# Kernel optimization log

Hardware: AMD Instinct MI355X
Metric: run time of the kernel (lower is better)

## Reference

```python
import jax, jax.numpy as jnp
import numpy as np

B, S, D = 2, 2048, 2048
H, KV, HD = 16, 8, 128
N_REP = H // KV


def _rotate_half(x):
    x1, x2 = x[..., : x.shape[-1] // 2], x[..., x.shape[-1] // 2 :]
    return jnp.concatenate((-x2, x1), axis=-1)


def setup_inputs() -> dict:
    key = jax.random.key(0)
    ks = jax.random.split(key, 5)
    x = jax.random.normal(ks[0], (B, S, D), dtype=jnp.float32)
    # rotary tables (llama-style): inv_freq over half dims, duplicated
    inv_freq = 1.0 / (10000.0 ** (jnp.arange(0, HD, 2, dtype=jnp.float32) / HD))
    t = jnp.arange(S, dtype=jnp.float32)
    freqs = jnp.outer(t, inv_freq)                      # [S, HD/2]
    emb = jnp.concatenate((freqs, freqs), axis=-1)      # [S, HD]
    cos, sin = jnp.cos(emb), jnp.sin(emb)
    sc = 0.02
    Wq = jax.random.normal(ks[1], (D, H * HD), dtype=jnp.float32) * sc
    Wk = jax.random.normal(ks[2], (D, KV * HD), dtype=jnp.float32) * sc
    Wv = jax.random.normal(ks[3], (D, KV * HD), dtype=jnp.float32) * sc
    Wo = jax.random.normal(ks[4], (H * HD, D), dtype=jnp.float32) * sc
    return {"x": x, "cos": cos, "sin": sin, "Wq": Wq, "Wk": Wk, "Wv": Wv, "Wo": Wo}


def reference(x, cos, sin, Wq, Wk, Wv, Wo):
    b, s, _ = x.shape
    q = (x @ Wq).reshape(b, s, H, HD)
    k = (x @ Wk).reshape(b, s, KV, HD)
    v = (x @ Wv).reshape(b, s, KV, HD)
    # RoPE (broadcast over batch and heads; unsqueeze_dim=2 layout [b,s,h,d])
    c = cos[None, :, None, :]
    sn = sin[None, :, None, :]
    q = q * c + _rotate_half(q) * sn
    k = k * c + _rotate_half(k) * sn
    # GQA expansion (repeat_kv == interleaved repeat along head dim)
    k = jnp.repeat(k, N_REP, axis=2)
    v = jnp.repeat(v, N_REP, axis=2)
    scale = HD ** -0.5
    # causal attention (single-rank ring attention == one causal flash block)
    scores = jnp.einsum("bqhd,bkhd->bhqk", q, k) * scale
    mask = jnp.tril(jnp.ones((s, s), dtype=bool))
    scores = jnp.where(mask[None, None], scores, -jnp.inf)
    probs = jax.nn.softmax(scores, axis=-1)
    attn = jnp.einsum("bhqk,bkhd->bqhd", probs, v).reshape(b, s, H * HD)
    return attn @ Wo
```

## Files before the change

kernel.cpp:

```cpp
#include <hip/hip_runtime.h>


typedef __bf16 bf16;
typedef __bf16 bf16x4 __attribute__((ext_vector_type(4)));
typedef __bf16 bf16x8 __attribute__((ext_vector_type(8)));
typedef float floatx4 __attribute__((ext_vector_type(4)));

#define AS1(p) ((const __attribute__((address_space(1))) void*)(p))
#define AS3(p) ((__attribute__((address_space(3))) void*)(p))

__device__ __forceinline__ void load16(const void* g, void* l) {
  __builtin_amdgcn_global_load_lds(AS1(g), AS3(l), 16, 0, 0);
}

__device__ __forceinline__ void phase_barrier() {
  asm volatile("" ::: "memory");
  __builtin_amdgcn_sched_barrier(0);
  __builtin_amdgcn_s_barrier();
  __builtin_amdgcn_sched_barrier(0);
  asm volatile("" ::: "memory");
}

__global__ __launch_bounds__(256) void cvt_kernel(const float* __restrict__ in,
                                                  bf16* __restrict__ out, int n4) {
  int i = blockIdx.x * blockDim.x + threadIdx.x;
  if (i >= n4) return;
  float4 v = ((const float4*)in)[i];
  bf16x4 o = {(bf16)v.x, (bf16)v.y, (bf16)v.z, (bf16)v.w};
  ((bf16x4*)out)[i] = o;
}

__global__ __launch_bounds__(256) void wtrans_kernel(
    const float* __restrict__ Wq, const float* __restrict__ Wk,
    const float* __restrict__ Wv, const float* __restrict__ Wo,
    bf16* __restrict__ WqkvT, bf16* __restrict__ WoT) {
  __shared__ float tile[32][33];
  const int wid = blockIdx.z;
  const float* src = wid == 0 ? Wq : wid == 1 ? Wk : wid == 2 ? Wv : Wo;
  bf16* dst = wid == 0 ? WqkvT
            : wid == 1 ? WqkvT + 2048ull * 2048
            : wid == 2 ? WqkvT + 3072ull * 2048
                       : WoT;
  const int ncols = (wid == 1 || wid == 2) ? 1024 : 2048;
  const int c0 = blockIdx.x * 32, r0 = blockIdx.y * 32;
  if (c0 >= ncols) return;
  const int tx = threadIdx.x & 31, ty = threadIdx.x >> 5;
#pragma unroll
  for (int i = 0; i < 4; i++) {
    int ri = ty + i * 8;
    tile[ri][tx] = src[(long)(r0 + ri) * ncols + c0 + tx];
  }
  __syncthreads();
#pragma unroll
  for (int i = 0; i < 4; i++) {
    int ci = ty + i * 8;
    dst[(long)(c0 + ci) * 2048 + r0 + tx] = (bf16)tile[tx][ci];
  }
}

__global__ __launch_bounds__(256) void transpose_bf16(
    const bf16* __restrict__ in, bf16* __restrict__ out,
    int ldi, int ldo, long ibs, long obs) {
  __shared__ bf16 tile[32][33];
  const long ib = ibs * blockIdx.z, ob = obs * blockIdx.z;
  const int c0 = blockIdx.x * 32, r0 = blockIdx.y * 32;
  const int tx = threadIdx.x & 31, ty = threadIdx.x >> 5;
#pragma unroll
  for (int i = 0; i < 4; i++) {
    int ri = ty + i * 8;
    tile[ri][tx] = in[ib + (long)(r0 + ri) * ldi + c0 + tx];
  }
  __syncthreads();
#pragma unroll
  for (int i = 0; i < 4; i++) {
    int ci = ty + i * 8;
    out[ob + (long)(c0 + ci) * ldo + r0 + tx] = tile[tx][ci];
  }
}

template <typename CT>
__global__ __launch_bounds__(512, 2) void gemm256(
    const bf16* __restrict__ A, const bf16* __restrict__ Bt, CT* __restrict__ C,
    int M, int N, int K) {
  __shared__ __align__(1024) char smem[131072];
  const int tid = threadIdx.x;
  const int wave = tid >> 6, lane = tid & 63;
  const int quad = lane >> 4, l16 = lane & 15;
  const int wm = wave >> 2, wn = wave & 3;
  const int m0 = blockIdx.y * 256, n0 = blockIdx.x * 256;

  const int srow = (wave >> 1) * 16 + (lane >> 2);
  const int skcol = (wave & 1) * 32 + (((lane & 3) * 8) ^ ((lane & 32) ? 16 : 0));
  const int sblk = wave * 1024;

  const int qoff = (quad * 16) ^ ((l16 & 8) << 2);
  const int aoff = wm * 16384 + l16 * 64 + qoff;
  const int boff = 32768 + (wn >> 1) * 16384 + (wn & 1) * 8192 + l16 * 64 + qoff;

  auto stageA = [&](int kt, int h, int buf) {
    const bf16* g = A + (size_t)(m0 + h * 128 + srow) * K + kt * 64 + skcol;
    char* d = smem + buf * 65536 + h * 16384 + sblk;
    load16(g, d);
    load16(g + (size_t)64 * K, d + 8192);
  };
  auto stageB = [&](int kt, int h, int buf) {
    const bf16* g = Bt + (size_t)(n0 + h * 128 + srow) * K + kt * 64 + skcol;
    char* d = smem + buf * 65536 + 32768 + h * 16384 + sblk;
    load16(g, d);
    load16(g + (size_t)64 * K, d + 8192);
  };
  auto rdA = [&](int buf, int fr, int ks) {
    return *(const bf16x8*)(smem + buf * 65536 + aoff + (fr * 2 + ks) * 1024);
  };
  auto rdB = [&](int buf, int fc, int ks) {
    return *(const bf16x8*)(smem + buf * 65536 + boff + (fc * 2 + ks) * 1024);
  };

  floatx4 acc[8][4] = {};

  const int nkt = K >> 6;
  const int niter = nkt >> 1;

  stageB(0, 0, 0); stageB(0, 1, 0);
  stageA(0, 0, 0); stageA(0, 1, 0);
  stageB(1, 0, 1); stageB(1, 1, 1);
  asm volatile("s_waitcnt vmcnt(4)" ::: "memory");
  phase_barrier();

  for (int it = 0; it < niter; ++it) {
    const int T = 2 * it;
    const bool morek = (it < niter - 1);
#pragma unroll
    for (int c = 0; c < 2; ++c) {
      const int buf = c;
      const int tA = T + 1 + c;
      const int tB = T + 2 + c;
      const bool stA = (c == 0) || morek;

      bf16x8 a[4][2], b01[2][2], b23[2][2];

#pragma unroll
      for (int fr = 0; fr < 4; ++fr)
#pragma unroll
        for (int ks = 0; ks < 2; ++ks) a[fr][ks] = rdA(buf, fr, ks);
#pragma unroll
      for (int fc = 0; fc < 2; ++fc)
#pragma unroll
        for (int ks = 0; ks < 2; ++ks) b01[fc][ks] = rdB(buf, fc, ks);
      if (stA) stageA(tA, 0, buf ^ 1);
      phase_barrier();
      __builtin_amdgcn_s_setprio(1);
#pragma unroll
      for (int ks = 0; ks < 2; ++ks)
#pragma unroll
        for (int fr = 0; fr < 4; ++fr)
#pragma unroll
          for (int fc = 0; fc < 2; ++fc)
            acc[fr][fc] = __builtin_amdgcn_mfma_f32_16x16x32_bf16(
                a[fr][ks], b01[fc][ks], acc[fr][fc], 0, 0, 0);
      __builtin_amdgcn_s_setprio(0);
      phase_barrier();

#pragma unroll
      for (int fc = 0; fc < 2; ++fc)
#pragma unroll
        for (int ks = 0; ks < 2; ++ks) b23[fc][ks] = rdB(buf, 2 + fc, ks);
      if (stA) stageA(tA, 1, buf ^ 1);
      phase_barrier();
      __builtin_amdgcn_s_setprio(1);
#pragma unroll
      for (int ks = 0; ks < 2; ++ks)
#pragma unroll
        for (int fr = 0; fr < 4; ++fr)
#pragma unroll
          for (int fc = 0; fc < 2; ++fc)
            acc[fr][2 + fc] = __builtin_amdgcn_mfma_f32_16x16x32_bf16(
                a[fr][ks], b23[fc][ks], acc[fr][2 + fc], 0, 0, 0);
      __builtin_amdgcn_s_setprio(0);
      phase_barrier();

#pragma unroll
      for (int fr = 0; fr < 4; ++fr)
#pragma unroll
        for (int ks = 0; ks < 2; ++ks) a[fr][ks] = rdA(buf, 4 + fr, ks);
      if (morek) stageB(tB, 0, buf);
      phase_barrier();
      __builtin_amdgcn_s_setprio(1);
#pragma unroll
      for (int ks = 0; ks < 2; ++ks)
#pragma unroll
        for (int fr = 0; fr < 4; ++fr)
#pragma unroll
          for (int fc = 0; fc < 2; ++fc)
            acc[4 + fr][2 + fc] = __builtin_amdgcn_mfma_f32_16x16x32_bf16(
                a[fr][ks], b23[fc][ks], acc[4 + fr][2 + fc], 0, 0, 0);
      __builtin_amdgcn_s_setprio(0);
      phase_barrier();

      if (morek) stageB(tB, 1, buf);
      if (morek)
        asm volatile("s_waitcnt vmcnt(4)" ::: "memory");
      else
        asm volatile("s_waitcnt vmcnt(0)" ::: "memory");
      phase_barrier();
      __builtin_amdgcn_s_setprio(1);
#pragma unroll
      for (int ks = 0; ks < 2; ++ks)
#pragma unroll
        for (int fr = 0; fr < 4; ++fr)
#pragma unroll
          for (int fc = 0; fc < 2; ++fc)
            acc[4 + fr][fc] = __builtin_amdgcn_mfma_f32_16x16x32_bf16(
                a[fr][ks], b01[fc][ks], acc[4 + fr][fc], 0, 0, 0);
      __builtin_amdgcn_s_setprio(0);
      phase_barrier();
    }
  }

#pragma unroll
  for (int fr = 0; fr < 8; ++fr)
#pragma unroll
    for (int fc = 0; fc < 4; ++fc)
#pragma unroll
      for (int r = 0; r < 4; ++r) {
        int row = m0 + wm * 128 + fr * 16 + quad * 4 + r;
        int col = n0 + wn * 64 + fc * 16 + l16;
        C[(size_t)row * N + col] = (CT)acc[fr][fc][r];
      }
}

__global__ void rope_kernel(bf16* __restrict__ QKV, const float* __restrict__ cosb,
                            const float* __restrict__ sinb) {
  int idx = blockIdx.x * blockDim.x + threadIdx.x;
  if (idx >= 6291456) return;
  int nh, nhs, offc;
  if (idx < 4194304) { nh = 16; nhs = 4; offc = 0; }
  else { idx -= 4194304; nh = 8; nhs = 3; offc = 2048; }
  int d = idx & 63;
  int rest = idx >> 6;
  int hh = rest & (nh - 1);
  int bs = rest >> nhs;
  int s = bs & 2047;
  size_t base = (size_t)bs * 4096 + offc + hh * 128;
  float c0 = cosb[s * 128 + d];
  float c1 = cosb[s * 128 + d + 64];
  float s0 = sinb[s * 128 + d];
  float s1 = sinb[s * 128 + d + 64];
  float x0 = (float)QKV[base + d];
  float x1 = (float)QKV[base + d + 64];
  QKV[base + d] = (bf16)(x0 * c0 - x1 * s0);
  QKV[base + d + 64] = (bf16)(x1 * c1 + x0 * s1);
}


template <bool MASK>
__device__ __forceinline__ void attn_step32(
    const bf16* Kc, const bf16* Vc, bf16* Pw, const bf16x8 (&aq)[4],
    const bf16x8& ones, floatx4 (&oacc)[8], floatx4& lacc,
    int k0, int q0w, int l16, int quad) {
  floatx4 sacc[4] = {};
  __builtin_amdgcn_s_setprio(1);
#pragma unroll
  for (int ks = 0; ks < 4; ks++)
#pragma unroll
    for (int j = 0; j < 4; j++) {
      int row = j * 16 + l16;
      bf16x8 bk = *(const bf16x8*)(Kc + row * 128 + (((ks * 4 + quad) ^ (row & 15)) * 8));
      sacc[j] = __builtin_amdgcn_mfma_f32_16x16x32_bf16(aq[ks], bk, sacc[j], 0, 0, 0);
    }
  __builtin_amdgcn_s_setprio(0);
  const float C = 0.12752188659023044f;
#pragma unroll
  for (int r = 0; r < 4; r++) {
    int row = quad * 4 + r;
#pragma unroll
    for (int j = 0; j < 4; j++) {
      float p = exp2f(sacc[j][r] * C);
      if (MASK) {
        int key = k0 + j * 16 + l16;
        if (key > q0w + row) p = 0.f;
      }
      int col = j * 16 + l16;
      Pw[row * 64 + (((col >> 3) ^ (row & 7)) * 8) + (col & 7)] = (bf16)p;
    }
  }
  __builtin_amdgcn_s_setprio(1);
#pragma unroll
  for (int ks = 0; ks < 2; ks++) {
    bf16x8 ap = *(const bf16x8*)(Pw + l16 * 64 + (((ks * 4 + quad) ^ (l16 & 7)) * 8));
    lacc = __builtin_amdgcn_mfma_f32_16x16x32_bf16(ap, ones, lacc, 0, 0, 0);
#pragma unroll
    for (int j = 0; j < 8; j++) {
      int vr = j * 16 + l16;
      bf16x8 bv = *(const bf16x8*)(Vc + vr * 64 + (((ks * 4 + quad) ^ (vr & 7)) * 8));
      oacc[j] = __builtin_amdgcn_mfma_f32_16x16x32_bf16(ap, bv, oacc[j], 0, 0, 0);
    }
  }
  __builtin_amdgcn_s_setprio(0);
}

__global__ __launch_bounds__(512, 4) void flash_kernel(
    const bf16* __restrict__ QKV, const bf16* __restrict__ Vt, bf16* __restrict__ O) {
  __shared__ __align__(1024) char smem[81920];
  const int tid = threadIdx.x;
  const int wave = tid >> 6, lane = tid & 63, quad = lane >> 4, l16 = lane & 15;
  const int wbase = tid & ~63;
  const int hloc = wave & 1, rgroup = wave >> 1;
  bf16* Pw = (bf16*)(smem + 65536) + wave * 1024;
  bf16x8 ones;
#pragma unroll
  for (int e = 0; e < 8; e++) ones[e] = (bf16)1.0f;

  const int w = blockIdx.x;
  const int side = w & 1, kvh = (w >> 1) & 7, b = (w >> 4) & 1, g = w >> 5;
  const int qt = side ? 31 - g : g;
  const int h = kvh * 2 + hloc;
  const int q0 = qt * 64;
  const int nkt = qt + 1;

#pragma unroll
  for (int u = 0; u < 4; u++) {
    int gg = u * 512 + tid;
    int row = gg >> 4, cc = gg & 15;
    const bf16* gp = QKV + (size_t)(b * 2048 + q0 + (row & 63)) * 4096 +
                     (kvh * 2 + (row >> 6)) * 128 + ((cc ^ (row & 15)) * 8);
    load16(gp, smem + (u * 512 + wbase) * 16);
  }
  asm volatile("s_waitcnt vmcnt(0)" ::: "memory");
  phase_barrier();
  bf16x8 aq[4];
  {
    int qr = hloc * 64 + rgroup * 16 + l16;
#pragma unroll
    for (int ks = 0; ks < 4; ks++)
      aq[ks] = *(const bf16x8*)((const bf16*)smem + qr * 128 +
                                (((ks * 4 + quad) ^ (qr & 15)) * 8));
  }
  __syncthreads();

  auto stageKV = [&](int kt, int nb) {
    char* kd = smem + nb * 16384;
    char* vd = smem + 32768 + nb * 16384;
#pragma unroll
    for (int u = 0; u < 2; u++) {
      int gg = u * 512 + tid;
      int krow = gg >> 4, kcc = gg & 15;
      const bf16* kp = QKV + (size_t)(b * 2048 + kt * 64 + krow) * 4096 + 2048 +
                       kvh * 128 + ((kcc ^ (krow & 15)) * 8);
      load16(kp, kd + (u * 512 + wbase) * 16);
      int vrow = gg >> 3, vcc = gg & 7;
      const bf16* vp = Vt + (size_t)(b * 1024 + kvh * 128 + vrow) * 2048 + kt * 64 +
                       ((vcc ^ (vrow & 7)) * 8);
      load16(vp, vd + (u * 512 + wbase) * 16);
    }
  };

  stageKV(0, 0);

  floatx4 oacc[8] = {};
  floatx4 lacc = {};
  const int q0w = q0 + rgroup * 16;

  for (int kt = 0; kt < nkt; kt++) {
    const int cur = kt & 1;
    if (kt + 1 < nkt) {
      stageKV(kt + 1, cur ^ 1);
      asm volatile("s_waitcnt vmcnt(4)" ::: "memory");
    } else {
      asm volatile("s_waitcnt vmcnt(0)" ::: "memory");
    }
    phase_barrier();
    const bf16* Kc = (const bf16*)(smem + cur * 16384);
    const bf16* Vc = (const bf16*)(smem + 32768 + cur * 16384);
    if (kt == nkt - 1)
      attn_step32<true>(Kc, Vc, Pw, aq, ones, oacc, lacc, kt * 64, q0w, l16, quad);
    else
      attn_step32<false>(Kc, Vc, Pw, aq, ones, oacc, lacc, kt * 64, q0w, l16, quad);
    phase_barrier();
  }

  float rl[4];
#pragma unroll
  for (int r = 0; r < 4; r++) rl[r] = 1.0f / lacc[r];
#pragma unroll
  for (int j = 0; j < 8; j++)
#pragma unroll
    for (int r = 0; r < 4; r++) {
      int s = q0w + quad * 4 + r;
      O[(size_t)(b * 2048 + s) * 2048 + h * 128 + j * 16 + l16] =
          (bf16)(oacc[j][r] * rl[r]);
    }
}

extern "C" void kernel_launch(void* const* d_in, const int* in_sizes, int n_in,
                              void* d_out, int out_size, void* d_ws, size_t ws_size,
                              hipStream_t stream) {
  (void)in_sizes; (void)n_in; (void)out_size; (void)ws_size;
  const float* x    = (const float*)d_in[0];
  const float* cosb = (const float*)d_in[1];
  const float* sinb = (const float*)d_in[2];
  const float* Wq   = (const float*)d_in[3];
  const float* Wk   = (const float*)d_in[4];
  const float* Wv   = (const float*)d_in[5];
  const float* Wo   = (const float*)d_in[6];
  float* out = (float*)d_out;

  char* ws = (char*)d_ws;
  size_t off = 0;
  auto alloc = [&](size_t bytes) { void* p = ws + off; off += bytes; return p; };
  bf16* xb    = (bf16*)alloc(4096ull * 2048 * 2);
  bf16* WqkvT = (bf16*)alloc(4096ull * 2048 * 2);
  bf16* WoT   = (bf16*)alloc(2048ull * 2048 * 2);
  bf16* QKV   = (bf16*)alloc(4096ull * 4096 * 2);
  bf16* Vtb   = (bf16*)alloc(2048ull * 2048 * 2);
  bf16* Ab    = (bf16*)alloc(4096ull * 2048 * 2);

  cvt_kernel<<<8192, 256, 0, stream>>>(x, xb, 2097152);

  wtrans_kernel<<<dim3(64, 64, 4), 256, 0, stream>>>(Wq, Wk, Wv, Wo, WqkvT, WoT);

  gemm256<bf16><<<dim3(16, 16), 512, 0, stream>>>(xb, WqkvT, QKV, 4096, 4096, 2048);

  rope_kernel<<<24576, 256, 0, stream>>>(QKV, cosb, sinb);

  transpose_bf16<<<dim3(32, 64, 2), 256, 0, stream>>>(
      QKV + 3072, Vtb, 4096, 2048, 2048ll * 4096, 1024ll * 2048);

  flash_kernel<<<dim3(512, 1, 1), 512, 0, stream>>>(QKV, Vtb, Ab);

  gemm256<float><<<dim3(8, 16), 512, 0, stream>>>(Ab, WoT, out, 4096, 2048, 2048);
}
```

Before: 342.1 us.

## Merge prep and mid kernels, use 256x128 tiles for output projection

Combines the x conversion and weight transpose into one launch, and RoPE plus the V transpose into another, which removes two kernel launches and their gaps. It also adds a 256x128-tile GEMM for the output projection, giving 256 blocks instead of 128 so more CUs are busy on the 4096x2048 output. The smaller tile lowers per-block data reuse and uses launch bounds of one block per CU.

```diff
diff --git a/kernel.cpp b/kernel.cpp
--- a/kernel.cpp
+++ b/kernel.cpp
@@ -21,28 +21,30 @@
   asm volatile("" ::: "memory");
 }
 
-__global__ __launch_bounds__(256) void cvt_kernel(const float* __restrict__ in,
-                                                  bf16* __restrict__ out, int n4) {
-  int i = blockIdx.x * blockDim.x + threadIdx.x;
-  if (i >= n4) return;
-  float4 v = ((const float4*)in)[i];
-  bf16x4 o = {(bf16)v.x, (bf16)v.y, (bf16)v.z, (bf16)v.w};
-  ((bf16x4*)out)[i] = o;
-}
-
-__global__ __launch_bounds__(256) void wtrans_kernel(
-    const float* __restrict__ Wq, const float* __restrict__ Wk,
-    const float* __restrict__ Wv, const float* __restrict__ Wo,
+__global__ __launch_bounds__(256) void prep_kernel(
+    const float* __restrict__ x, const float* __restrict__ Wq,
+    const float* __restrict__ Wk, const float* __restrict__ Wv,
+    const float* __restrict__ Wo, bf16* __restrict__ xb,
     bf16* __restrict__ WqkvT, bf16* __restrict__ WoT) {
   __shared__ float tile[32][33];
-  const int wid = blockIdx.z;
+  const int bi = blockIdx.x;
+  if (bi < 8192) {
+    int i = bi * 256 + threadIdx.x;
+    float4 v = ((const float4*)x)[i];
+    bf16x4 o = {(bf16)v.x, (bf16)v.y, (bf16)v.z, (bf16)v.w};
+    ((bf16x4*)xb)[i] = o;
+    return;
+  }
+  const int i2 = bi - 8192;
+  const int wid = i2 >> 12;
+  const int r0 = ((i2 >> 6) & 63) * 32;
+  const int c0 = (i2 & 63) * 32;
   const float* src = wid == 0 ? Wq : wid == 1 ? Wk : wid == 2 ? Wv : Wo;
   bf16* dst = wid == 0 ? WqkvT
             : wid == 1 ? WqkvT + 2048ull * 2048
             : wid == 2 ? WqkvT + 3072ull * 2048
                        : WoT;
   const int ncols = (wid == 1 || wid == 2) ? 1024 : 2048;
-  const int c0 = blockIdx.x * 32, r0 = blockIdx.y * 32;
   if (c0 >= ncols) return;
   const int tx = threadIdx.x & 31, ty = threadIdx.x >> 5;
 #pragma unroll
@@ -58,23 +60,49 @@
   }
 }
 
-__global__ __launch_bounds__(256) void transpose_bf16(
-    const bf16* __restrict__ in, bf16* __restrict__ out,
-    int ldi, int ldo, long ibs, long obs) {
+__global__ __launch_bounds__(256) void mid_kernel(
+    bf16* __restrict__ QKV, const float* __restrict__ cosb,
+    const float* __restrict__ sinb, bf16* __restrict__ Vtb) {
   __shared__ bf16 tile[32][33];
-  const long ib = ibs * blockIdx.z, ob = obs * blockIdx.z;
-  const int c0 = blockIdx.x * 32, r0 = blockIdx.y * 32;
+  const int bi = blockIdx.x;
+  if (bi < 24576) {
+    int idx = bi * 256 + threadIdx.x;
+    int nh, nhs, offc;
+    if (idx < 4194304) { nh = 16; nhs = 4; offc = 0; }
+    else { idx -= 4194304; nh = 8; nhs = 3; offc = 2048; }
+    int d = idx & 63;
+    int rest = idx >> 6;
+    int hh = rest & (nh - 1);
+    int bs = rest >> nhs;
+    int s = bs & 2047;
+    size_t base = (size_t)bs * 4096 + offc + hh * 128;
+    float c0 = cosb[s * 128 + d];
+    float c1 = cosb[s * 128 + d + 64];
+    float s0 = sinb[s * 128 + d];
+    float s1 = sinb[s * 128 + d + 64];
+    float x0 = (float)QKV[base + d];
+    float x1 = (float)QKV[base + d + 64];
+    QKV[base + d] = (bf16)(x0 * c0 - x1 * s0);
+    QKV[base + d + 64] = (bf16)(x1 * c1 + x0 * s1);
+    return;
+  }
+  const int i2 = bi - 24576;
+  const int z = i2 >> 11;
+  const int r0 = ((i2 >> 5) & 63) * 32;
+  const int c0 = (i2 & 31) * 32;
+  const bf16* in = QKV + 3072;
+  const long ib = 2048ll * 4096 * z, ob = 1024ll * 2048 * z;
   const int tx = threadIdx.x & 31, ty = threadIdx.x >> 5;
 #pragma unroll
   for (int i = 0; i < 4; i++) {
     int ri = ty + i * 8;
-    tile[ri][tx] = in[ib + (long)(r0 + ri) * ldi + c0 + tx];
+    tile[ri][tx] = in[ib + (long)(r0 + ri) * 4096 + c0 + tx];
   }
   __syncthreads();
 #pragma unroll
   for (int i = 0; i < 4; i++) {
     int ci = ty + i * 8;
-    out[ob + (long)(c0 + ci) * ldo + r0 + tx] = tile[tx][ci];
+    Vtb[ob + (long)(c0 + ci) * 2048 + r0 + tx] = tile[tx][ci];
   }
 }
 
@@ -229,29 +257,156 @@
       }
 }
 
-__global__ void rope_kernel(bf16* __restrict__ QKV, const float* __restrict__ cosb,
-                            const float* __restrict__ sinb) {
-  int idx = blockIdx.x * blockDim.x + threadIdx.x;
-  if (idx >= 6291456) return;
-  int nh, nhs, offc;
-  if (idx < 4194304) { nh = 16; nhs = 4; offc = 0; }
-  else { idx -= 4194304; nh = 8; nhs = 3; offc = 2048; }
-  int d = idx & 63;
-  int rest = idx >> 6;
-  int hh = rest & (nh - 1);
-  int bs = rest >> nhs;
-  int s = bs & 2047;
-  size_t base = (size_t)bs * 4096 + offc + hh * 128;
-  float c0 = cosb[s * 128 + d];
-  float c1 = cosb[s * 128 + d + 64];
-  float s0 = sinb[s * 128 + d];
-  float s1 = sinb[s * 128 + d + 64];
-  float x0 = (float)QKV[base + d];
-  float x1 = (float)QKV[base + d + 64];
-  QKV[base + d] = (bf16)(x0 * c0 - x1 * s0);
-  QKV[base + d + 64] = (bf16)(x1 * c1 + x0 * s1);
-}
-
+__global__ __launch_bounds__(512, 1) void gemm256x128(
+    const bf16* __restrict__ A, const bf16* __restrict__ Bt, float* __restrict__ C,
+    int M, int N, int K) {
+  __shared__ __align__(1024) char smem[98304];
+  const int tid = threadIdx.x;
+  const int wave = tid >> 6, lane = tid & 63;
+  const int quad = lane >> 4, l16 = lane & 15;
+  const int wm = wave >> 1, wn = wave & 1;
+  const int m0 = blockIdx.y * 256, n0 = blockIdx.x * 128;
+
+  const int srow = (wave >> 1) * 16 + (lane >> 2);
+  const int skcol = (wave & 1) * 32 + (((lane & 3) * 8) ^ ((lane & 32) ? 16 : 0));
+  const int sblk = wave * 1024;
+
+  const int qoff = (quad * 16) ^ ((l16 & 8) << 2);
+  const int aoff = (wm >> 1) * 16384 + l16 * 64 + qoff;
+  const int afrag = (wm & 1) * 4;
+  const int boff = 32768 + l16 * 64 + qoff;
+  const int bfrag = wn * 4;
+
+  auto stageA = [&](int kt, int h, int buf) {
+    const bf16* g = A + (size_t)(m0 + h * 128 + srow) * K + kt * 64 + skcol;
+    char* d = smem + buf * 49152 + h * 16384 + sblk;
+    load16(g, d);
+    load16(g + (size_t)64 * K, d + 8192);
+  };
+  auto stageB = [&](int kt, int buf) {
+    const bf16* g = Bt + (size_t)(n0 + srow) * K + kt * 64 + skcol;
+    char* d = smem + buf * 49152 + 32768 + sblk;
+    load16(g, d);
+    load16(g + (size_t)64 * K, d + 8192);
+  };
+  auto rdA = [&](int buf, int fr, int ks) {
+    return *(const bf16x8*)(smem + buf * 49152 + aoff + ((afrag + fr) * 2 + ks) * 1024);
+  };
+  auto rdB = [&](int buf, int fc, int ks) {
+    return *(const bf16x8*)(smem + buf * 49152 + boff + ((bfrag + fc) * 2 + ks) * 1024);
+  };
+
+  floatx4 acc[4][4] = {};
+
+  const int nkt = K >> 6;
+  const int niter = nkt >> 1;
+
+  stageB(0, 0);
+  stageA(0, 0, 0); stageA(0, 1, 0);
+  stageB(1, 1);
+  asm volatile("s_waitcnt vmcnt(2)" ::: "memory");
+  phase_barrier();
+
+  for (int it = 0; it < niter; ++it) {
+    const int T = 2 * it;
+    const bool morek = (it < niter - 1);
+#pragma unroll
+    for (int c = 0; c < 2; ++c) {
+      const int buf = c;
+      const int tA = T + 1 + c;
+      const int tB = T + 2 + c;
+      const bool stA = (c == 0) || morek;
+
+      bf16x8 a[2][2], b01[2][2], b23[2][2];
+
+#pragma unroll
+      for (int fr = 0; fr < 2; ++fr)
+#pragma unroll
+        for (int ks = 0; ks < 2; ++ks) a[fr][ks] = rdA(buf, fr, ks);
+#pragma unroll
+      for (int fc = 0; fc < 2; ++fc)
+#pragma unroll
+        for (int ks = 0; ks < 2; ++ks) b01[fc][ks] = rdB(buf, fc, ks);
+      if (stA) stageA(tA, 0, buf ^ 1);
+      phase_barrier();
+      __builtin_amdgcn_s_setprio(1);
+#pragma unroll
+      for (int ks = 0; ks < 2; ++ks)
+#pragma unroll
+        for (int fr = 0; fr < 2; ++fr)
+#pragma unroll
+          for (int fc = 0; fc < 2; ++fc)
+            acc[fr][fc] = __builtin_amdgcn_mfma_f32_16x16x32_bf16(
+                a[fr][ks], b01[fc][ks], acc[fr][fc], 0, 0, 0);
+      __builtin_amdgcn_s_setprio(0);
+      phase_barrier();
+
+#pragma unroll
+      for (int fc = 0; fc < 2; ++fc)
+#pragma unroll
+        for (int ks = 0; ks < 2; ++ks) b23[fc][ks] = rdB(buf, 2 + fc, ks);
+      if (stA) stageA(tA, 1, buf ^ 1);
+      phase_barrier();
+      __builtin_amdgcn_s_setprio(1);
+#pragma unroll
+      for (int ks = 0; ks < 2; ++ks)
+#pragma unroll
+        for (int fr = 0; fr < 2; ++fr)
+#pragma unroll
+          for (int fc = 0; fc < 2; ++fc)
+            acc[fr][2 + fc] = __builtin_amdgcn_mfma_f32_16x16x32_bf16(
+                a[fr][ks], b23[fc][ks], acc[fr][2 + fc], 0, 0, 0);
+      __builtin_amdgcn_s_setprio(0);
+      phase_barrier();
+
+#pragma unroll
+      for (int fr = 0; fr < 2; ++fr)
+#pragma unroll
+        for (int ks = 0; ks < 2; ++ks) a[fr][ks] = rdA(buf, 2 + fr, ks);
+      if (morek) stageB(tB, buf);
+      phase_barrier();
+      __builtin_amdgcn_s_setprio(1);
+#pragma unroll
+      for (int ks = 0; ks < 2; ++ks)
+#pragma unroll
+        for (int fr = 0; fr < 2; ++fr)
+#pragma unroll
+          for (int fc = 0; fc < 2; ++fc)
+            acc[2 + fr][2 + fc] = __builtin_amdgcn_mfma_f32_16x16x32_bf16(
+                a[fr][ks], b23[fc][ks], acc[2 + fr][2 + fc], 0, 0, 0);
+      __builtin_amdgcn_s_setprio(0);
+      phase_barrier();
+
+      if (morek)
+        asm volatile("s_waitcnt vmcnt(2)" ::: "memory");
+      else
+        asm volatile("s_waitcnt vmcnt(0)" ::: "memory");
+      phase_barrier();
+      __builtin_amdgcn_s_setprio(1);
+#pragma unroll
+      for (int ks = 0; ks < 2; ++ks)
+#pragma unroll
+        for (int fr = 0; fr < 2; ++fr)
+#pragma unroll
+          for (int fc = 0; fc < 2; ++fc)
+            acc[2 + fr][fc] = __builtin_amdgcn_mfma_f32_16x16x32_bf16(
+                a[fr][ks], b01[fc][ks], acc[2 + fr][fc], 0, 0, 0);
+      __builtin_amdgcn_s_setprio(0);
+      phase_barrier();
+    }
+  }
+
+#pragma unroll
+  for (int fr = 0; fr < 4; ++fr)
+#pragma unroll
+    for (int fc = 0; fc < 4; ++fc)
+#pragma unroll
+      for (int r = 0; r < 4; ++r) {
+        int row = m0 + wm * 64 + fr * 16 + quad * 4 + r;
+        int col = n0 + wn * 64 + fc * 16 + l16;
+        C[(size_t)row * N + col] = acc[fr][fc][r];
+      }
+}
 
 template <bool MASK>
 __device__ __forceinline__ void attn_step32(
@@ -415,18 +570,13 @@
   bf16* Vtb   = (bf16*)alloc(2048ull * 2048 * 2);
   bf16* Ab    = (bf16*)alloc(4096ull * 2048 * 2);
 
-  cvt_kernel<<<8192, 256, 0, stream>>>(x, xb, 2097152);
-
-  wtrans_kernel<<<dim3(64, 64, 4), 256, 0, stream>>>(Wq, Wk, Wv, Wo, WqkvT, WoT);
+  prep_kernel<<<8192 + 16384, 256, 0, stream>>>(x, Wq, Wk, Wv, Wo, xb, WqkvT, WoT);
 
   gemm256<bf16><<<dim3(16, 16), 512, 0, stream>>>(xb, WqkvT, QKV, 4096, 4096, 2048);
 
-  rope_kernel<<<24576, 256, 0, stream>>>(QKV, cosb, sinb);
-
-  transpose_bf16<<<dim3(32, 64, 2), 256, 0, stream>>>(
-      QKV + 3072, Vtb, 4096, 2048, 2048ll * 4096, 1024ll * 2048);
+  mid_kernel<<<24576 + 4096, 256, 0, stream>>>(QKV, cosb, sinb, Vtb);
 
   flash_kernel<<<dim3(512, 1, 1), 512, 0, stream>>>(QKV, Vtb, Ab);
 
-  gemm256<float><<<dim3(8, 16), 512, 0, stream>>>(Ab, WoT, out, 4096, 2048, 2048);
-}
+  gemm256x128<<<dim3(16, 16), 512, 0, stream>>>(Ab, WoT, out, 4096, 2048, 2048);
+}
```

New measurement: 317.6 us. 7.2% less time.
